# Kernel tuning notes

Measured on AMD Instinct MI355X. Metric: run time of the kernel, lower is better.

Reference implementation:

```python
import jax, jax.numpy as jnp
import numpy as np

EPS_RMS = 1e-8
EPS_LN = 1e-5


def _rms(x):
    return x / jnp.sqrt(jnp.mean(x * x, axis=-1, keepdims=True) + EPS_RMS)


def _ln(x, g, b):
    m = jnp.mean(x, axis=-1, keepdims=True)
    v = jnp.mean((x - m) ** 2, axis=-1, keepdims=True)
    return (x - m) / jnp.sqrt(v + EPS_LN) * g + b


def setup_inputs() -> dict:
    B, S, D, K, V, F = 2, 256, 1024, 8, 32000, 2048
    key = jax.random.key(0)
    ks = jax.random.split(key, 12)
    s = 0.02

    def n(k, shape):
        return jax.random.normal(k, shape, dtype=jnp.float32) * s

    return {
        "x": jax.random.randint(ks[0], (B, S), 0, V),
        "embed_table": n(ks[1], (V, D)),
        "unembed_w": n(ks[2], (V, D)),
        "proj_w": n(ks[3], (K, D, 2 * D)),
        "proj_b": jnp.zeros((K, D), jnp.float32),
        "sa_wv": n(ks[4], (K, D, D)),
        "sa_bv": jnp.zeros((K, D), jnp.float32),
        "sa_wo": n(ks[5], (K, D, D)),
        "sa_bo": jnp.zeros((K, D), jnp.float32),
        "ln1_g": jnp.ones((K, D), jnp.float32),
        "ln1_b": jnp.zeros((K, D), jnp.float32),
        "ca_wv": n(ks[6], (K, D, D)),
        "ca_bv": jnp.zeros((K, D), jnp.float32),
        "ca_wo": n(ks[7], (K, D, D)),
        "ca_bo": jnp.zeros((K, D), jnp.float32),
        "ln2_g": jnp.ones((K, D), jnp.float32),
        "ln2_b": jnp.zeros((K, D), jnp.float32),
        "ff_w1": n(ks[8], (K, F, D)),
        "ff_b1": jnp.zeros((K, F), jnp.float32),
        "ff_w2": n(ks[9], (K, D, F)),
        "ff_b2": jnp.zeros((K, D), jnp.float32),
        "ln3_g": jnp.ones((K, D), jnp.float32),
        "ln3_b": jnp.zeros((K, D), jnp.float32),
    }


def reference(x, embed_table, unembed_w, proj_w, proj_b,
              sa_wv, sa_bv, sa_wo, sa_bo, ln1_g, ln1_b,
              ca_wv, ca_bv, ca_wo, ca_bo, ln2_g, ln2_b,
              ff_w1, ff_b1, ff_w2, ff_b2, ln3_g, ln3_b):
    K = proj_w.shape[0]
    emb = embed_table[x]                      # [B, S, D]
    B, S, D = emb.shape
    I = S - K                                 # number of outer positions (max_i + 1)
    h = emb[:, :I, :]                         # h_prev for all start positions, [B, I, D]
    logits_k = []
    for k in range(K):
        e = emb[:, k + 1:k + 1 + I, :]        # future token embeds for head k
        merged = jnp.concatenate([_rms(h), _rms(e)], axis=-1)   # [B, I, 2D]
        xp = jnp.einsum('bid,ed->bie', merged, proj_w[k]) + proj_b[k]
        # TransformerDecoderLayer on a length-1 sequence: softmax over a single
        # key == 1, so (self-/cross-)attention reduces to out_proj(v_proj(.)).
        sa = (xp @ sa_wv[k].T + sa_bv[k]) @ sa_wo[k].T + sa_bo[k]
        x1 = _ln(xp + sa, ln1_g[k], ln1_b[k])
        ca = (xp @ ca_wv[k].T + ca_bv[k]) @ ca_wo[k].T + ca_bo[k]   # memory = layer input
        x2 = _ln(x1 + ca, ln2_g[k], ln2_b[k])
        ff = jax.nn.relu(x2 @ ff_w1[k].T + ff_b1[k]) @ ff_w2[k].T + ff_b2[k]
        x3 = _ln(x2 + ff, ln3_g[k], ln3_b[k])
        logits_k.append(x3 @ unembed_w.T)     # [B, I, V]
        h = x3
    return jnp.stack(logits_k, axis=2)        # [B, I, K, V]
```

## Files before the change

### kernel.cpp

```cpp
#include <hip/hip_runtime.h>
#include <hip/hip_bf16.h>

#define Dd 1024
#define Ss 256
#define Bz 2
#define Kk 8
#define Vv 32000
#define Ff 2048
#define Ii 248
#define Mm (Bz*Ii)
#define Mp 512
#define Mu (Kk*Mm)
#define Mx 4096

typedef __attribute__((ext_vector_type(8))) short bf16x8_t;
typedef __attribute__((ext_vector_type(4))) float f32x4_t;
typedef __attribute__((ext_vector_type(16))) float f32x16_t;
typedef unsigned long long u64;

__device__ inline ushort f2b(float f) {
    union { float f; unsigned u; } v; v.f = f;
    unsigned u = v.u;
    unsigned r = (u + 0x7fffu + ((u >> 16) & 1u)) >> 16;
    return (ushort)r;
}

__device__ inline void gload16(const void* g, void* l) {
    __builtin_amdgcn_global_load_lds((const __attribute__((address_space(1))) void*)g,
                                     (__attribute__((address_space(3))) void*)l, 16, 0, 0);
}

template<int N> __device__ inline void wait_vmcnt() {
    asm volatile("s_waitcnt vmcnt(%0)" :: "n"(N) : "memory");
}
__device__ inline void bar() {
    asm volatile("" ::: "memory");
    __builtin_amdgcn_s_barrier();
    asm volatile("" ::: "memory");
}

template<int BK>
__device__ inline int swz(int s, int r) {
    if constexpr (BK == 64) return s ^ (r & 7);
    else                    return s ^ ((r >> 1) & 3);
}

__global__ __launch_bounds__(512, 2)
void gemm32(const ushort* __restrict__ A, const ushort* __restrict__ W,
            float* __restrict__ Cf, int Mrows, int KDIM) {
    constexpr int BM = 256, BN = 256, BK = 64, TH = 512, PF = 2;
    constexpr int TILE = (BM + BN) * BK;
    constexpr int ABYTES = BM * BK * 2;
    constexpr int L = (BM + BN) * BK * 2 / (TH * 16);
    __shared__ __align__(16) ushort sm[PF * TILE];

    int bx = blockIdx.x, by = blockIdx.y;
    {
        const int nwg  = gridDim.x * gridDim.y;
        const int orig = by * gridDim.x + bx;
        const int q = nwg >> 3, r = nwg & 7;
        const int xcd = orig & 7, lin = orig >> 3;
        const int wg = (xcd < r ? xcd * (q + 1) : r * (q + 1) + (xcd - r) * q) + lin;
        bx = wg % gridDim.x; by = wg / gridDim.x;
    }
    const int t    = threadIdx.x;
    const int lane = t & 63;
    const int w    = t >> 6;
    const int wr   = (w >> 2) * 128;
    const int wc   = (w & 3) * 64;
    const int tm0  = bx * BM, tn0 = by * BN;

    const ushort* Abase = A + (size_t)tm0 * KDIM;
    const ushort* Wbase = W + (size_t)tn0 * KDIM;

    const ushort* gp[L]; int lo[L];
    #pragma unroll
    for (int j = 0; j < L; ++j) {
        const int i = (t + j * TH) * 16;
        int r, s; const ushort* base;
        if (i < ABYTES) { r = i / (BK * 2); s = (i >> 4) % (BK / 8); base = Abase; }
        else { const int i2 = i - ABYTES; r = i2 / (BK * 2); s = (i2 >> 4) % (BK / 8); base = Wbase; }
        gp[j] = base + (size_t)r * KDIM + (size_t)swz<BK>(s, r) * 8;
        lo[j] = i / 2;
    }
    auto stage = [&](int buf) {
        #pragma unroll
        for (int j = 0; j < L; ++j) gload16(gp[j], &sm[buf * TILE + lo[j]]);
        #pragma unroll
        for (int j = 0; j < L; ++j) gp[j] += BK;
    };

    const int rl = lane & 31, hk = lane >> 5;
    int aoff[4][4], boff[2][4];
    #pragma unroll
    for (int m = 0; m < 4; ++m)
        #pragma unroll
        for (int ks = 0; ks < 4; ++ks) {
            const int r = wr + m * 32 + rl;
            aoff[m][ks] = r * BK + swz<BK>(ks * 2 + hk, r) * 8;
        }
    #pragma unroll
    for (int n = 0; n < 2; ++n)
        #pragma unroll
        for (int ks = 0; ks < 4; ++ks) {
            const int r = wc + n * 32 + rl;
            boff[n][ks] = BM * BK + r * BK + swz<BK>(ks * 2 + hk, r) * 8;
        }

    f32x16_t acc[4][2] = {};
    const int NT = KDIM / BK;

    stage(0); stage(1);
    int buf = 0;
    for (int kt = 0; kt < NT; ++kt) {
        const int remT = NT - 1 - kt;
        if (remT >= 1) wait_vmcnt<L>(); else wait_vmcnt<0>();
        bar();

        const ushort* smb = &sm[buf * TILE];
        #pragma unroll
        for (int ks = 0; ks < 4; ++ks) {
            bf16x8_t af[4], bf[2];
            #pragma unroll
            for (int m = 0; m < 4; ++m) af[m] = *(const bf16x8_t*)&smb[aoff[m][ks]];
            #pragma unroll
            for (int n = 0; n < 2; ++n) bf[n] = *(const bf16x8_t*)&smb[boff[n][ks]];
            #pragma unroll
            for (int m = 0; m < 4; ++m)
                #pragma unroll
                for (int n = 0; n < 2; ++n)
                    acc[m][n] = __builtin_amdgcn_mfma_f32_32x32x16_bf16(af[m], bf[n], acc[m][n], 0, 0, 0);
        }
        bar();
        if (kt + PF < NT) stage(buf);
        buf ^= 1;
    }

    const int cl = lane & 31;
    #pragma unroll
    for (int m = 0; m < 4; ++m)
        #pragma unroll
        for (int n = 0; n < 2; ++n)
            #pragma unroll
            for (int reg = 0; reg < 16; ++reg) {
                const int row = (reg & 3) + 8 * (reg >> 2) + 4 * hk;
                const int r = tm0 + wr + m * 32 + row;
                const int c = tn0 + wc + n * 32 + cl;
                if (r < Mrows) {
                    const int kk  = r / Mm;
                    const int rem = r - kk * Mm;
                    Cf[(size_t)(rem * Kk + kk) * Vv + c] = acc[m][n][reg];
                }
            }
}

template<int BM, int BN, int BK, int TH, int PF, bool RELU, bool UNEMBED>
__global__ __launch_bounds__(TH, 2)
void gemm3(const ushort* __restrict__ A0, const ushort* __restrict__ A1, int lda,
           const ushort* __restrict__ W0, const ushort* __restrict__ W1,
           const float* __restrict__ b0, const float* __restrict__ b1,
           float* __restrict__ Cf0, float* __restrict__ Cf1,
           ushort* __restrict__ Cb0, ushort* __restrict__ Cb1,
           int Mrows, int N, int KDIM) {
    constexpr int NW = TH / 64;
    constexpr int WN = NW / 2;
    constexpr int MR = (BM / 2) / 16;
    constexpr int NR = (BN / WN) / 16;
    constexpr int TILE = (BM + BN) * BK;
    constexpr int ABYTES = BM * BK * 2;
    constexpr int TOT = (BM + BN) * BK * 2;
    constexpr int L = TOT / (TH * 16);
    constexpr int KS = BK / 32;

    __shared__ __align__(16) ushort sm[PF * TILE];

    const ushort* A = A0; const ushort* W = W0; const float* bias = b0;
    float* Cf = Cf0; ushort* Cb = Cb0;
    if (blockIdx.z) { A = A1; W = W1; bias = b1; Cf = Cf1; Cb = Cb1; }

    const int t    = threadIdx.x;
    const int tm0  = blockIdx.x * BM;
    const int tn0  = blockIdx.y * BN;
    const int lane = t & 63;
    const int w    = t >> 6;
    const int wr   = (w / WN) * (BM / 2);
    const int wc   = (w % WN) * (BN / WN);

    const ushort* Abase = A + (size_t)tm0 * lda;
    const ushort* Wbase = W + (size_t)tn0 * KDIM;

    const ushort* gp[L];
    int lo[L];
    #pragma unroll
    for (int j = 0; j < L; ++j) {
        const int i = (t + j * TH) * 16;
        int r, s; const ushort* base; int ld;
        if (i < ABYTES) { r = i / (BK * 2); s = (i >> 4) % (BK / 8); base = Abase; ld = lda; }
        else { const int i2 = i - ABYTES; r = i2 / (BK * 2); s = (i2 >> 4) % (BK / 8); base = Wbase; ld = KDIM; }
        gp[j] = base + (size_t)r * ld + swz<BK>(s, r) * 8;
        lo[j] = i / 2;
    }
    auto stage = [&](int buf) {
        #pragma unroll
        for (int j = 0; j < L; ++j) gload16(gp[j], &sm[buf * TILE + lo[j]]);
        #pragma unroll
        for (int j = 0; j < L; ++j) gp[j] += BK;
    };

    const int h = lane >> 4, rl = lane & 15;
    int aoff[MR][KS], boff[NR][KS];
    #pragma unroll
    for (int m = 0; m < MR; ++m)
        #pragma unroll
        for (int kk = 0; kk < KS; ++kk) {
            const int r = wr + m * 16 + rl;
            aoff[m][kk] = r * BK + swz<BK>(kk * 4 + h, r) * 8;
        }
    #pragma unroll
    for (int n = 0; n < NR; ++n)
        #pragma unroll
        for (int kk = 0; kk < KS; ++kk) {
            const int r = wc + n * 16 + rl;
            boff[n][kk] = BM * BK + r * BK + swz<BK>(kk * 4 + h, r) * 8;
        }

    f32x4_t acc[MR][NR] = {};

    const int NT = KDIM / BK;
    #pragma unroll
    for (int p = 0; p < PF; ++p) stage(p);

    int buf = 0;
    for (int kt = 0; kt < NT; ++kt) {
        const int remT = NT - 1 - kt;
        const int wv = remT < PF - 1 ? remT : PF - 1;
        switch (wv) {
            case 0:  wait_vmcnt<0>();     break;
            case 1:  wait_vmcnt<1 * L>(); break;
            case 2:  wait_vmcnt<2 * L>(); break;
            default: wait_vmcnt<3 * L>(); break;
        }
        bar();

        const ushort* smb = &sm[buf * TILE];
        #pragma unroll
        for (int kk = 0; kk < KS; ++kk) {
            bf16x8_t af[MR], bf[NR];
            #pragma unroll
            for (int m = 0; m < MR; ++m) af[m] = *(const bf16x8_t*)&smb[aoff[m][kk]];
            #pragma unroll
            for (int n = 0; n < NR; ++n) bf[n] = *(const bf16x8_t*)&smb[boff[n][kk]];
            #pragma unroll
            for (int m = 0; m < MR; ++m)
                #pragma unroll
                for (int n = 0; n < NR; ++n)
                    acc[m][n] = __builtin_amdgcn_mfma_f32_16x16x32_bf16(af[m], bf[n], acc[m][n], 0, 0, 0);
        }
        bar();
        if (kt + PF < NT) stage(buf);
        buf = (buf + 1 == PF) ? 0 : buf + 1;
    }

    const int rb = (lane >> 4) * 4;
    const int cl = lane & 15;
    #pragma unroll
    for (int m = 0; m < MR; ++m)
        #pragma unroll
        for (int n = 0; n < NR; ++n)
            #pragma unroll
            for (int i = 0; i < 4; ++i) {
                const int r = tm0 + wr + m * 16 + rb + i;
                const int c = tn0 + wc + n * 16 + cl;
                if (r < Mrows) {
                    float v = acc[m][n][i];
                    if (bias) v += bias[c];
                    if (RELU) v = fmaxf(v, 0.f);
                    if (UNEMBED) {
                        const int kk  = r / Mm;
                        const int rem = r - kk * Mm;
                        Cf[(size_t)(rem * Kk + kk) * Vv + c] = v;
                    } else {
                        if (Cf) Cf[(size_t)r * N + c] = v;
                        if (Cb) Cb[(size_t)r * N + c] = f2b(v);
                    }
                }
            }
}

__global__ __launch_bounds__(256)
void convert_k(const float* __restrict__ src, ushort* __restrict__ dst,
               long n, long perK, long dstPerK, long dstOff) {
    long i = ((long)blockIdx.x * 256 + threadIdx.x) * 4;
    const long stride = (long)gridDim.x * 1024;
    for (; i < n; i += stride) {
        const float4 v = *(const float4*)(src + i);
        const long k = i / perK, rem = i - k * perK;
        ushort4 hh; hh.x = f2b(v.x); hh.y = f2b(v.y); hh.z = f2b(v.z); hh.w = f2b(v.w);
        *(ushort4*)(dst + k * dstPerK + dstOff + rem) = hh;
    }
}

__global__ __launch_bounds__(256)
void copyf_k(const float* __restrict__ src, float* __restrict__ dst,
             long n, long perK, long dstPerK, long dstOff) {
    long i = (long)blockIdx.x * 256 + threadIdx.x;
    const long stride = (long)gridDim.x * 256;
    for (; i < n; i += stride) {
        const long k = i / perK, rem = i - k * perK;
        dst[k * dstPerK + dstOff + rem] = src[i];
    }
}


__global__ __launch_bounds__(256)
void ln12_kernel(const float* __restrict__ sa, const float* __restrict__ xp,
                 const float* __restrict__ ca,
                 const float* __restrict__ g1, const float* __restrict__ b1,
                 const float* __restrict__ g2, const float* __restrict__ b2,
                 float* __restrict__ x2f, ushort* __restrict__ x2b) {
    __shared__ float reds[16];
    const int row = blockIdx.x;
    const int t = threadIdx.x;
    const float4 va = *(const float4*)(sa + (size_t)row * Dd + t * 4);
    const float4 vp = *(const float4*)(xp + (size_t)row * Dd + t * 4);
    float x[4] = { va.x + vp.x, va.y + vp.y, va.z + vp.z, va.w + vp.w };
    float s = x[0] + x[1] + x[2] + x[3];
    float q = x[0]*x[0] + x[1]*x[1] + x[2]*x[2] + x[3]*x[3];
    for (int m = 32; m; m >>= 1) { s += __shfl_xor(s, m); q += __shfl_xor(q, m); }
    if ((t & 63) == 0) { reds[t >> 6] = s; reds[4 + (t >> 6)] = q; }
    __syncthreads();
    s = reds[0] + reds[1] + reds[2] + reds[3];
    q = reds[4] + reds[5] + reds[6] + reds[7];
    float mean = s * (1.f / Dd);
    float rstd = rsqrtf(q * (1.f / Dd) - mean * mean + 1e-5f);
    const float4 vc = *(const float4*)(ca + (size_t)row * Dd + t * 4);
    float y[4];
    #pragma unroll
    for (int j = 0; j < 4; ++j) {
        const int c = t * 4 + j;
        y[j] = (x[j] - mean) * rstd * g1[c] + b1[c] + ((const float*)&vc)[j];
    }
    s = y[0] + y[1] + y[2] + y[3];
    q = y[0]*y[0] + y[1]*y[1] + y[2]*y[2] + y[3]*y[3];
    for (int m = 32; m; m >>= 1) { s += __shfl_xor(s, m); q += __shfl_xor(q, m); }
    if ((t & 63) == 0) { reds[8 + (t >> 6)] = s; reds[12 + (t >> 6)] = q; }
    __syncthreads();
    s = reds[8] + reds[9] + reds[10] + reds[11];
    q = reds[12] + reds[13] + reds[14] + reds[15];
    mean = s * (1.f / Dd);
    rstd = rsqrtf(q * (1.f / Dd) - mean * mean + 1e-5f);
    float z[4]; ushort4 hb;
    #pragma unroll
    for (int j = 0; j < 4; ++j) {
        const int c = t * 4 + j;
        z[j] = (y[j] - mean) * rstd * g2[c] + b2[c];
    }
    hb.x = f2b(z[0]); hb.y = f2b(z[1]); hb.z = f2b(z[2]); hb.w = f2b(z[3]);
    *(float4*)(x2f + (size_t)row * Dd + t * 4) = make_float4(z[0], z[1], z[2], z[3]);
    *(ushort4*)(x2b + (size_t)row * Dd + t * 4) = hb;
}

__global__ __launch_bounds__(256)
void ln3m_kernel(const float* __restrict__ ff, const float* __restrict__ x2,
                 const float* __restrict__ g3, const float* __restrict__ b3,
                 const ushort* __restrict__ remb, ushort* __restrict__ x3k,
                 ushort* __restrict__ merged, int k) {
    __shared__ float reds[12];
    const int r = blockIdx.x;
    const int t = threadIdx.x;
    const int b = r / Ii, i = r - b * Ii;
    const float4 vf = *(const float4*)(ff + (size_t)r * Dd + t * 4);
    const float4 v2 = *(const float4*)(x2 + (size_t)r * Dd + t * 4);
    float x[4] = { vf.x + v2.x, vf.y + v2.y, vf.z + v2.z, vf.w + v2.w };
    float s = x[0] + x[1] + x[2] + x[3];
    float q = x[0]*x[0] + x[1]*x[1] + x[2]*x[2] + x[3]*x[3];
    for (int m = 32; m; m >>= 1) { s += __shfl_xor(s, m); q += __shfl_xor(q, m); }
    if ((t & 63) == 0) { reds[t >> 6] = s; reds[4 + (t >> 6)] = q; }
    __syncthreads();
    s = reds[0] + reds[1] + reds[2] + reds[3];
    q = reds[4] + reds[5] + reds[6] + reds[7];
    const float mean = s * (1.f / Dd);
    const float rstd = rsqrtf(q * (1.f / Dd) - mean * mean + 1e-5f);
    float y[4];
    #pragma unroll
    for (int j = 0; j < 4; ++j) {
        const int c = t * 4 + j;
        y[j] = (x[j] - mean) * rstd * g3[c] + b3[c];
    }
    ushort4 hy; hy.x = f2b(y[0]); hy.y = f2b(y[1]); hy.z = f2b(y[2]); hy.w = f2b(y[3]);
    *(ushort4*)(x3k + (size_t)r * Dd + t * 4) = hy;
    float q2 = y[0]*y[0] + y[1]*y[1] + y[2]*y[2] + y[3]*y[3];
    for (int m = 32; m; m >>= 1) q2 += __shfl_xor(q2, m);
    if ((t & 63) == 0) reds[8 + (t >> 6)] = q2;
    __syncthreads();
    if (k + 1 < Kk) {
        q2 = reds[8] + reds[9] + reds[10] + reds[11];
        const float sc = rsqrtf(q2 * (1.f / Dd) + 1e-8f);
        ushort4 hm; hm.x = f2b(y[0]*sc); hm.y = f2b(y[1]*sc); hm.z = f2b(y[2]*sc); hm.w = f2b(y[3]*sc);
        *(ushort4*)(merged + (size_t)r * (2 * Dd) + t * 4) = hm;
        const ushort4 ev = *(const ushort4*)(remb + (size_t)(b * Ss + k + 2 + i) * Dd + t * 4);
        *(ushort4*)(merged + (size_t)r * (2 * Dd) + Dd + t * 4) = ev;
    }
}

__global__ __launch_bounds__(256)
void gather_rms_merged(const int* __restrict__ xi, const float* __restrict__ table,
                       ushort* __restrict__ remb, ushort* __restrict__ merged) {
    __shared__ float reds[4];
    const int row = blockIdx.x;
    const int t = threadIdx.x;
    const int idx = xi[row];
    const float4 xv = *(const float4*)(table + (size_t)idx * Dd + t * 4);
    float q = xv.x*xv.x + xv.y*xv.y + xv.z*xv.z + xv.w*xv.w;
    for (int m = 32; m; m >>= 1) q += __shfl_xor(q, m);
    if ((t & 63) == 0) reds[t >> 6] = q;
    __syncthreads();
    q = reds[0] + reds[1] + reds[2] + reds[3];
    const float sc = rsqrtf(q * (1.f / Dd) + 1e-8f);
    ushort4 h;
    h.x = f2b(xv.x * sc); h.y = f2b(xv.y * sc); h.z = f2b(xv.z * sc); h.w = f2b(xv.w * sc);
    *(ushort4*)(remb + (size_t)row * Dd + t * 4) = h;
    const int b = row / Ss, s2 = row - b * Ss;
    if (s2 < Ii)
        *(ushort4*)(merged + (size_t)(b * Ii + s2) * (2 * Dd) + t * 4) = h;
    if (s2 >= 1 && s2 <= Ii)
        *(ushort4*)(merged + (size_t)(b * Ii + s2 - 1) * (2 * Dd) + Dd + t * 4) = h;
}


__device__ inline bf16x8_t ld_frag(const ushort* p) {
    union { u64 l[2]; bf16x8_t s; } u;
    u.l[0] = *(const u64*)p;
    u.l[1] = *(const u64*)(p + 4);
    return u.s;
}

#define LDST 40

template<int KDIM, bool RELU, bool UNEMBED>
__global__ __launch_bounds__(256)
void gemm64(const ushort* __restrict__ A, const float* __restrict__ Wt,
            const float* __restrict__ bias, float* __restrict__ Cf,
            ushort* __restrict__ Cb, int Mrows, int N) {
    __shared__ ushort As[64 * LDST];
    __shared__ ushort Ws[64 * LDST];
    const int t    = threadIdx.x;
    const int tm0  = blockIdx.x * 64;
    const int tn0  = blockIdx.y * 64;
    const int lr   = t >> 2;
    const int lc   = (t & 3) * 8;
    const int wid  = t >> 6;
    const int lane = t & 63;
    const int wr   = (wid >> 1) * 32;
    const int wc   = (wid & 1) * 32;
    f32x4_t acc[2][2] = {};
    const bool avalid = (tm0 + lr) < Mrows;
    const ushort* Ap = A  + (size_t)(tm0 + lr) * KDIM + lc;
    const float*  Wp = Wt + (size_t)(tn0 + lr) * KDIM + lc;
    const int aoff = lr * LDST + lc;

    for (int k0 = 0; k0 < KDIM; k0 += 32) {
        union { uint4 qv; u64 l[2]; } av;
        av.qv = make_uint4(0u, 0u, 0u, 0u);
        if (avalid) av.qv = *(const uint4*)(Ap + k0);
        const float4 w0 = *(const float4*)(Wp + k0);
        const float4 w1 = *(const float4*)(Wp + k0 + 4);
        union { ushort us[8]; u64 l[2]; } wb;
        wb.us[0] = f2b(w0.x); wb.us[1] = f2b(w0.y); wb.us[2] = f2b(w0.z); wb.us[3] = f2b(w0.w);
        wb.us[4] = f2b(w1.x); wb.us[5] = f2b(w1.y); wb.us[6] = f2b(w1.z); wb.us[7] = f2b(w1.w);
        __syncthreads();
        *(u64*)&As[aoff]     = av.l[0];
        *(u64*)&As[aoff + 4] = av.l[1];
        *(u64*)&Ws[aoff]     = wb.l[0];
        *(u64*)&Ws[aoff + 4] = wb.l[1];
        __syncthreads();

        const ushort* ab = &As[(wr + (lane & 15)) * LDST + (lane >> 4) * 8];
        const ushort* bb = &Ws[(wc + (lane & 15)) * LDST + (lane >> 4) * 8];
        const bf16x8_t fa0 = ld_frag(ab);
        const bf16x8_t fa1 = ld_frag(ab + 16 * LDST);
        const bf16x8_t fb0 = ld_frag(bb);
        const bf16x8_t fb1 = ld_frag(bb + 16 * LDST);
        acc[0][0] = __builtin_amdgcn_mfma_f32_16x16x32_bf16(fa0, fb0, acc[0][0], 0, 0, 0);
        acc[0][1] = __builtin_amdgcn_mfma_f32_16x16x32_bf16(fa0, fb1, acc[0][1], 0, 0, 0);
        acc[1][0] = __builtin_amdgcn_mfma_f32_16x16x32_bf16(fa1, fb0, acc[1][0], 0, 0, 0);
        acc[1][1] = __builtin_amdgcn_mfma_f32_16x16x32_bf16(fa1, fb1, acc[1][1], 0, 0, 0);
    }

    const int rb = (lane >> 4) * 4;
    const int cl = lane & 15;
    for (int m = 0; m < 2; ++m)
        for (int n = 0; n < 2; ++n)
            for (int i = 0; i < 4; ++i) {
                const int r = tm0 + wr + m * 16 + rb + i;
                const int c = tn0 + wc + n * 16 + cl;
                if (r < Mrows) {
                    float v = acc[m][n][i];
                    if (bias) v += bias[c];
                    if (RELU) v = fmaxf(v, 0.f);
                    if (UNEMBED) {
                        const int kk  = r / Mm;
                        const int rem = r - kk * Mm;
                        Cf[(size_t)(rem * Kk + kk) * Vv + c] = v;
                    } else {
                        if (Cf) Cf[(size_t)r * N + c] = v;
                        if (Cb) Cb[(size_t)r * N + c] = f2b(v);
                    }
                }
            }
}

__global__ __launch_bounds__(256)
void ln_kernel(const float* __restrict__ a, const float* __restrict__ rsd,
               const float* __restrict__ g, const float* __restrict__ bb,
               float* __restrict__ outf, ushort* __restrict__ outb) {
    __shared__ float reds[8];
    const int row = blockIdx.x;
    const int t = threadIdx.x;
    const float4 xa = *(const float4*)(a   + (size_t)row * Dd + t * 4);
    const float4 xr = *(const float4*)(rsd + (size_t)row * Dd + t * 4);
    float x[4] = { xa.x + xr.x, xa.y + xr.y, xa.z + xr.z, xa.w + xr.w };
    float s = x[0] + x[1] + x[2] + x[3];
    float q = x[0]*x[0] + x[1]*x[1] + x[2]*x[2] + x[3]*x[3];
    for (int msk = 32; msk; msk >>= 1) { s += __shfl_xor(s, msk); q += __shfl_xor(q, msk); }
    if ((t & 63) == 0) { reds[t >> 6] = s; reds[4 + (t >> 6)] = q; }
    __syncthreads();
    s = reds[0] + reds[1] + reds[2] + reds[3];
    q = reds[4] + reds[5] + reds[6] + reds[7];
    const float m    = s * (1.f / Dd);
    const float var  = q * (1.f / Dd) - m * m;
    const float rstd = rsqrtf(var + 1e-5f);
    float y[4];
    #pragma unroll
    for (int j = 0; j < 4; ++j) {
        const int c = t * 4 + j;
        y[j] = (x[j] - m) * rstd * g[c] + bb[c];
    }
    if (outf) *(float4*)(outf + (size_t)row * Dd + t * 4) = make_float4(y[0], y[1], y[2], y[3]);
    if (outb) {
        ushort4 h; h.x = f2b(y[0]); h.y = f2b(y[1]); h.z = f2b(y[2]); h.w = f2b(y[3]);
        *(ushort4*)(outb + (size_t)row * Dd + t * 4) = h;
    }
}

__global__ __launch_bounds__(256)
void build_merged(const float* __restrict__ h, const ushort* __restrict__ remb,
                  ushort* __restrict__ merged, int k) {
    __shared__ float reds[4];
    const int r = blockIdx.x;
    const int t = threadIdx.x;
    const int b = r / Ii;
    const int i = r - b * Ii;
    if (k == 0) {
        const ushort4 hv = *(const ushort4*)(remb + (size_t)(b * Ss + i) * Dd + t * 4);
        *(ushort4*)(merged + (size_t)r * (2 * Dd) + t * 4) = hv;
    } else {
        const float4 xv = *(const float4*)(h + (size_t)r * Dd + t * 4);
        float q = xv.x*xv.x + xv.y*xv.y + xv.z*xv.z + xv.w*xv.w;
        for (int msk = 32; msk; msk >>= 1) q += __shfl_xor(q, msk);
        if ((t & 63) == 0) reds[t >> 6] = q;
        __syncthreads();
        q = reds[0] + reds[1] + reds[2] + reds[3];
        const float sc = rsqrtf(q * (1.f / Dd) + 1e-8f);
        ushort4 hv;
        hv.x = f2b(xv.x * sc); hv.y = f2b(xv.y * sc); hv.z = f2b(xv.z * sc); hv.w = f2b(xv.w * sc);
        *(ushort4*)(merged + (size_t)r * (2 * Dd) + t * 4) = hv;
    }
    const ushort4 ev = *(const ushort4*)(remb + (size_t)(b * Ss + k + 1 + i) * Dd + t * 4);
    *(ushort4*)(merged + (size_t)r * (2 * Dd) + Dd + t * 4) = ev;
}

__global__ __launch_bounds__(256)
void gather_rms(const int* __restrict__ xi, const float* __restrict__ table,
                ushort* __restrict__ remb) {
    __shared__ float reds[4];
    const int row = blockIdx.x;
    const int t = threadIdx.x;
    const int idx = xi[row];
    const float4 xv = *(const float4*)(table + (size_t)idx * Dd + t * 4);
    float q = xv.x*xv.x + xv.y*xv.y + xv.z*xv.z + xv.w*xv.w;
    for (int msk = 32; msk; msk >>= 1) q += __shfl_xor(q, msk);
    if ((t & 63) == 0) reds[t >> 6] = q;
    __syncthreads();
    q = reds[0] + reds[1] + reds[2] + reds[3];
    const float sc = rsqrtf(q * (1.f / Dd) + 1e-8f);
    ushort4 h;
    h.x = f2b(xv.x * sc); h.y = f2b(xv.y * sc); h.z = f2b(xv.z * sc); h.w = f2b(xv.w * sc);
    *(ushort4*)(remb + (size_t)row * Dd + t * 4) = h;
}


extern "C" void kernel_launch(void* const* d_in, const int* in_sizes, int n_in,
                              void* d_out, int out_size, void* d_ws, size_t ws_size,
                              hipStream_t stream) {
    const int*   x      = (const int*)  d_in[0];
    const float* table  = (const float*)d_in[1];
    const float* unemb  = (const float*)d_in[2];
    const float* proj_w = (const float*)d_in[3];
    const float* proj_b = (const float*)d_in[4];
    const float* sa_wv  = (const float*)d_in[5];
    const float* sa_bv  = (const float*)d_in[6];
    const float* sa_wo  = (const float*)d_in[7];
    const float* sa_bo  = (const float*)d_in[8];
    const float* ln1_g  = (const float*)d_in[9];
    const float* ln1_b  = (const float*)d_in[10];
    const float* ca_wv  = (const float*)d_in[11];
    const float* ca_bv  = (const float*)d_in[12];
    const float* ca_wo  = (const float*)d_in[13];
    const float* ca_bo  = (const float*)d_in[14];
    const float* ln2_g  = (const float*)d_in[15];
    const float* ln2_b  = (const float*)d_in[16];
    const float* ff_w1  = (const float*)d_in[17];
    const float* ff_b1  = (const float*)d_in[18];
    const float* ff_w2  = (const float*)d_in[19];
    const float* ff_b2  = (const float*)d_in[20];
    const float* ln3_g  = (const float*)d_in[21];
    const float* ln3_b  = (const float*)d_in[22];
    float* out = (float*)d_out;

    char* ws = (char*)d_ws;
    size_t off = 0;
    auto alloc = [&](size_t bytes) -> void* {
        void* p = ws + off;
        off = (off + bytes + 255) & ~(size_t)255;
        return p;
    };

    const size_t NEED = 262100000;

    if (ws_size >= NEED) {
        ushort* wU  = (ushort*)alloc((size_t)Vv * Dd * 2);
        ushort* wP  = (ushort*)alloc((size_t)Kk * Dd * 2 * Dd * 2);
        ushort* wV  = (ushort*)alloc((size_t)Kk * 2 * Dd * Dd * 2);
        ushort* wOs = (ushort*)alloc((size_t)Kk * Dd * Dd * 2);
        ushort* wOc = (ushort*)alloc((size_t)Kk * Dd * Dd * 2);
        ushort* wF1 = (ushort*)alloc((size_t)Kk * Ff * Dd * 2);
        ushort* wF2 = (ushort*)alloc((size_t)Kk * Dd * Ff * 2);
        float*  bV  = (float*) alloc((size_t)Kk * 2 * Dd * 4);
        ushort* remb   = (ushort*)alloc((size_t)Bz * Ss * Dd * 2);
        ushort* merged = (ushort*)alloc((size_t)Mp * 2 * Dd * 2);
        float*  xpf    = (float*) alloc((size_t)Mp * Dd * 4);
        ushort* xpb    = (ushort*)alloc((size_t)Mp * Dd * 2);
        ushort* tb     = (ushort*)alloc((size_t)Mp * 2 * Dd * 2);
        float*  sfa    = (float*) alloc((size_t)Mp * Dd * 4);
        float*  sfc    = (float*) alloc((size_t)Mp * Dd * 4);
        float*  x2f    = (float*) alloc((size_t)Mp * Dd * 4);
        ushort* x2b    = (ushort*)alloc((size_t)Mp * Dd * 2);
        ushort* x3all  = (ushort*)alloc((size_t)Mx * Dd * 2);

        const long nU = (long)Vv * Dd;
        convert_k<<<2048, 256, 0, stream>>>(unemb, wU, nU, nU, nU, 0);
        const long nP = (long)Kk * Dd * 2 * Dd;
        convert_k<<<2048, 256, 0, stream>>>(proj_w, wP, nP, nP, nP, 0);
        const long nDD = (long)Kk * Dd * Dd, pDD = (long)Dd * Dd, pV = 2 * pDD;
        convert_k<<<2048, 256, 0, stream>>>(sa_wv, wV, nDD, pDD, pV, 0);
        convert_k<<<2048, 256, 0, stream>>>(ca_wv, wV, nDD, pDD, pV, pDD);
        convert_k<<<2048, 256, 0, stream>>>(sa_wo, wOs, nDD, nDD, nDD, 0);
        convert_k<<<2048, 256, 0, stream>>>(ca_wo, wOc, nDD, nDD, nDD, 0);
        const long nF = (long)Kk * Ff * Dd;
        convert_k<<<2048, 256, 0, stream>>>(ff_w1, wF1, nF, nF, nF, 0);
        convert_k<<<2048, 256, 0, stream>>>(ff_w2, wF2, nF, nF, nF, 0);
        copyf_k<<<32, 256, 0, stream>>>(sa_bv, bV, (long)Kk * Dd, Dd, 2 * Dd, 0);
        copyf_k<<<32, 256, 0, stream>>>(ca_bv, bV, (long)Kk * Dd, Dd, 2 * Dd, Dd);

        gather_rms_merged<<<Bz * Ss, 256, 0, stream>>>(x, table, remb, merged);

        for (int k = 0; k < Kk; ++k) {
            gemm3<32, 64, 64, 256, 3, false, false><<<dim3(Mp/32, Dd/64, 1), 256, 0, stream>>>(
                merged, merged, 2 * Dd, wP + (size_t)k * Dd * 2 * Dd, wP + (size_t)k * Dd * 2 * Dd,
                proj_b + k * Dd, proj_b + k * Dd, xpf, xpf, xpb, xpb, Mm, Dd, 2 * Dd);
            gemm3<32, 64, 64, 256, 3, false, false><<<dim3(Mp/32, 2*Dd/64, 1), 256, 0, stream>>>(
                xpb, xpb, Dd, wV + (size_t)k * pV, wV + (size_t)k * pV,
                bV + (size_t)k * 2 * Dd, bV + (size_t)k * 2 * Dd,
                nullptr, nullptr, tb, tb, Mm, 2 * Dd, Dd);
            gemm3<32, 64, 64, 256, 3, false, false><<<dim3(Mp/32, Dd/64, 2), 256, 0, stream>>>(
                tb, tb + Dd, 2 * Dd, wOs + (size_t)k * pDD, wOc + (size_t)k * pDD,
                sa_bo + k * Dd, ca_bo + k * Dd, sfa, sfc, nullptr, nullptr, Mm, Dd, Dd);
            ln12_kernel<<<Mm, 256, 0, stream>>>(sfa, xpf, sfc,
                ln1_g + k * Dd, ln1_b + k * Dd, ln2_g + k * Dd, ln2_b + k * Dd, x2f, x2b);
            gemm3<32, 64, 64, 256, 3, true, false><<<dim3(Mp/32, Ff/64, 1), 256, 0, stream>>>(
                x2b, x2b, Dd, wF1 + (size_t)k * Ff * Dd, wF1 + (size_t)k * Ff * Dd,
                ff_b1 + k * Ff, ff_b1 + k * Ff, nullptr, nullptr, tb, tb, Mm, Ff, Dd);
            gemm3<32, 64, 64, 256, 3, false, false><<<dim3(Mp/32, Dd/64, 1), 256, 0, stream>>>(
                tb, tb, Ff, wF2 + (size_t)k * Dd * Ff, wF2 + (size_t)k * Dd * Ff,
                ff_b2 + k * Dd, ff_b2 + k * Dd, sfa, sfa, nullptr, nullptr, Mm, Dd, Ff);
            ln3m_kernel<<<Mm, 256, 0, stream>>>(sfa, x2f, ln3_g + k * Dd, ln3_b + k * Dd,
                remb, x3all + (size_t)k * Mm * Dd, merged, k);
        }

        gemm32<<<dim3(Mx/256, Vv/256, 1), 512, 0, stream>>>(x3all, wU, out, Mu, Dd);
        return;
    }

    ushort* remb   = (ushort*)alloc((size_t)Bz * Ss * Dd * 2);
    ushort* merged = (ushort*)alloc((size_t)Mm * 2 * Dd * 2);
    float*  xpf    = (float*) alloc((size_t)Mm * Dd * 4);
    ushort* xpb    = (ushort*)alloc((size_t)Mm * Dd * 2);
    ushort* tb     = (ushort*)alloc((size_t)Mm * Ff * 2);
    float*  sf     = (float*) alloc((size_t)Mm * Dd * 4);
    float*  x1f    = (float*) alloc((size_t)Mm * Dd * 4);
    float*  x2f    = (float*) alloc((size_t)Mm * Dd * 4);
    ushort* x2b    = (ushort*)alloc((size_t)Mm * Dd * 2);
    float*  hbuf   = (float*) alloc((size_t)Mm * Dd * 4);
    ushort* x3all  = (ushort*)alloc((size_t)Kk * Mm * Dd * 2);

    gather_rms<<<Bz * Ss, 256, 0, stream>>>(x, table, remb);

    const dim3 gD((Mm + 63) / 64, Dd / 64);
    const dim3 gF((Mm + 63) / 64, Ff / 64);
    for (int k = 0; k < Kk; ++k) {
        build_merged<<<Mm, 256, 0, stream>>>(hbuf, remb, merged, k);
        gemm64<2 * Dd, false, false><<<gD, 256, 0, stream>>>(
            merged, proj_w + (size_t)k * Dd * 2 * Dd, proj_b + k * Dd, xpf, xpb, Mm, Dd);
        gemm64<Dd, false, false><<<gD, 256, 0, stream>>>(
            xpb, sa_wv + (size_t)k * Dd * Dd, sa_bv + k * Dd, nullptr, tb, Mm, Dd);
        gemm64<Dd, false, false><<<gD, 256, 0, stream>>>(
            tb, sa_wo + (size_t)k * Dd * Dd, sa_bo + k * Dd, sf, nullptr, Mm, Dd);
        ln_kernel<<<Mm, 256, 0, stream>>>(sf, xpf, ln1_g + k * Dd, ln1_b + k * Dd, x1f, nullptr);
        gemm64<Dd, false, false><<<gD, 256, 0, stream>>>(
            xpb, ca_wv + (size_t)k * Dd * Dd, ca_bv + k * Dd, nullptr, tb, Mm, Dd);
        gemm64<Dd, false, false><<<gD, 256, 0, stream>>>(
            tb, ca_wo + (size_t)k * Dd * Dd, ca_bo + k * Dd, sf, nullptr, Mm, Dd);
        ln_kernel<<<Mm, 256, 0, stream>>>(sf, x1f, ln2_g + k * Dd, ln2_b + k * Dd, x2f, x2b);
        gemm64<Dd, true, false><<<gF, 256, 0, stream>>>(
            x2b, ff_w1 + (size_t)k * Ff * Dd, ff_b1 + k * Ff, nullptr, tb, Mm, Ff);
        gemm64<Ff, false, false><<<gD, 256, 0, stream>>>(
            tb, ff_w2 + (size_t)k * Dd * Ff, ff_b2 + k * Dd, sf, nullptr, Mm, Dd);
        ln_kernel<<<Mm, 256, 0, stream>>>(sf, x2f, ln3_g + k * Dd, ln3_b + k * Dd,
                                          hbuf, x3all + (size_t)k * Mm * Dd);
    }

    const dim3 gU((Kk * Mm) / 64, Vv / 64);
    gemm64<Dd, false, true><<<gU, 256, 0, stream>>>(x3all, unemb, nullptr, out, nullptr, Kk * Mm, Vv);
}
```

Measured before the change: 990.4 us.

## Piggyback weight fp32-to-bf16 conversion as rider blocks on per-layer GEMM launches

```diff
diff --git a/kernel.cpp b/kernel.cpp
--- a/kernel.cpp
+++ b/kernel.cpp
@@ -45,6 +45,163 @@
     else                    return s ^ ((r >> 1) & 3);
 }
 
+#define NTASK 52
+struct CvTab {
+    u64 src[NTASK];
+    u64 dst[NTASK];
+    int start[NTASK + 1];
+    int n;
+};
+
+__device__ inline void run_rider(const CvTab& tab, int g) {
+    int lo = 0;
+    while (lo + 1 < tab.n && tab.start[lo + 1] <= g) ++lo;
+    const float* s = (const float*)tab.src[lo];
+    ushort* d = (ushort*)tab.dst[lo];
+    const long e0 = (long)(g - tab.start[lo]) * 4096 + threadIdx.x * 16;
+    #pragma unroll
+    for (int j = 0; j < 4; ++j) {
+        const float4 v = *(const float4*)(s + e0 + j * 4);
+        ushort4 h; h.x = f2b(v.x); h.y = f2b(v.y); h.z = f2b(v.z); h.w = f2b(v.w);
+        *(ushort4*)(d + e0 + j * 4) = h;
+    }
+}
+
+template<int BM, int BN, int BK, int TH, int PF, int MINW, bool RELU>
+__global__ __launch_bounds__(TH, MINW)
+void gemm3(const ushort* __restrict__ A0, const ushort* __restrict__ A1, int lda,
+           const ushort* __restrict__ W0, const ushort* __restrict__ W1,
+           const float* __restrict__ b0, const float* __restrict__ b1,
+           float* __restrict__ Cf0, float* __restrict__ Cf1,
+           ushort* __restrict__ Cb0, ushort* __restrict__ Cb1,
+           int Mrows, int N, int KDIM,
+           int zChain, CvTab tab, int rBase, int rCnt) {
+    constexpr int NW = TH / 64;
+    constexpr int WN = NW / 2;
+    constexpr int MR = (BM / 2) / 16;
+    constexpr int NR = (BN / WN) / 16;
+    constexpr int TILE = (BM + BN) * BK;
+    constexpr int ABYTES = BM * BK * 2;
+    constexpr int TOT = (BM + BN) * BK * 2;
+    constexpr int L = TOT / (TH * 16);
+    constexpr int KS = BK / 32;
+
+    __shared__ __align__(16) ushort sm[PF * TILE];
+
+    if ((int)blockIdx.z >= zChain) {
+        const int ord = (blockIdx.z - zChain) * (gridDim.x * gridDim.y)
+                      + blockIdx.y * gridDim.x + blockIdx.x;
+        if (ord < rCnt) run_rider(tab, rBase + ord);
+        return;
+    }
+
+    const ushort* A = A0; const ushort* W = W0; const float* bias = b0;
+    float* Cf = Cf0; ushort* Cb = Cb0;
+    if (blockIdx.z) { A = A1; W = W1; bias = b1; Cf = Cf1; Cb = Cb1; }
+
+    const int t    = threadIdx.x;
+    const int tm0  = blockIdx.x * BM;
+    const int tn0  = blockIdx.y * BN;
+    const int lane = t & 63;
+    const int w    = t >> 6;
+    const int wr   = (w / WN) * (BM / 2);
+    const int wc   = (w % WN) * (BN / WN);
+
+    const ushort* Abase = A + (size_t)tm0 * lda;
+    const ushort* Wbase = W + (size_t)tn0 * KDIM;
+
+    const ushort* gp[L];
+    int lo[L];
+    #pragma unroll
+    for (int j = 0; j < L; ++j) {
+        const int i = (t + j * TH) * 16;
+        int r, s; const ushort* base; int ld;
+        if (i < ABYTES) { r = i / (BK * 2); s = (i >> 4) % (BK / 8); base = Abase; ld = lda; }
+        else { const int i2 = i - ABYTES; r = i2 / (BK * 2); s = (i2 >> 4) % (BK / 8); base = Wbase; ld = KDIM; }
+        gp[j] = base + (size_t)r * ld + swz<BK>(s, r) * 8;
+        lo[j] = i / 2;
+    }
+    auto stage = [&](int buf) {
+        #pragma unroll
+        for (int j = 0; j < L; ++j) gload16(gp[j], &sm[buf * TILE + lo[j]]);
+        #pragma unroll
+        for (int j = 0; j < L; ++j) gp[j] += BK;
+    };
+
+    const int h = lane >> 4, rl = lane & 15;
+    int aoff[MR][KS], boff[NR][KS];
+    #pragma unroll
+    for (int m = 0; m < MR; ++m)
+        #pragma unroll
+        for (int kk = 0; kk < KS; ++kk) {
+            const int r = wr + m * 16 + rl;
+            aoff[m][kk] = r * BK + swz<BK>(kk * 4 + h, r) * 8;
+        }
+    #pragma unroll
+    for (int n = 0; n < NR; ++n)
+        #pragma unroll
+        for (int kk = 0; kk < KS; ++kk) {
+            const int r = wc + n * 16 + rl;
+            boff[n][kk] = BM * BK + r * BK + swz<BK>(kk * 4 + h, r) * 8;
+        }
+
+    f32x4_t acc[MR][NR] = {};
+
+    const int NT = KDIM / BK;
+    #pragma unroll
+    for (int p = 0; p < PF; ++p) stage(p);
+
+    int buf = 0;
+    for (int kt = 0; kt < NT; ++kt) {
+        const int remT = NT - 1 - kt;
+        const int wv = remT < PF - 1 ? remT : PF - 1;
+        switch (wv) {
+            case 0:  wait_vmcnt<0>();     break;
+            case 1:  wait_vmcnt<1 * L>(); break;
+            case 2:  wait_vmcnt<2 * L>(); break;
+            default: wait_vmcnt<3 * L>(); break;
+        }
+        bar();
+
+        const ushort* smb = &sm[buf * TILE];
+        #pragma unroll
+        for (int kk = 0; kk < KS; ++kk) {
+            bf16x8_t af[MR], bf[NR];
+            #pragma unroll
+            for (int m = 0; m < MR; ++m) af[m] = *(const bf16x8_t*)&smb[aoff[m][kk]];
+            #pragma unroll
+            for (int n = 0; n < NR; ++n) bf[n] = *(const bf16x8_t*)&smb[boff[n][kk]];
+            #pragma unroll
+            for (int m = 0; m < MR; ++m)
+                #pragma unroll
+                for (int n = 0; n < NR; ++n)
+                    acc[m][n] = __builtin_amdgcn_mfma_f32_16x16x32_bf16(af[m], bf[n], acc[m][n], 0, 0, 0);
+        }
+        bar();
+        if (kt + PF < NT) stage(buf);
+        buf = (buf + 1 == PF) ? 0 : buf + 1;
+    }
+
+    const int rb = (lane >> 4) * 4;
+    const int cl = lane & 15;
+    #pragma unroll
+    for (int m = 0; m < MR; ++m)
+        #pragma unroll
+        for (int n = 0; n < NR; ++n)
+            #pragma unroll
+            for (int i = 0; i < 4; ++i) {
+                const int r = tm0 + wr + m * 16 + rb + i;
+                const int c = tn0 + wc + n * 16 + cl;
+                if (r < Mrows) {
+                    float v = acc[m][n][i];
+                    if (bias) v += bias[c];
+                    if (RELU) v = fmaxf(v, 0.f);
+                    if (Cf) Cf[(size_t)r * N + c] = v;
+                    if (Cb) Cb[(size_t)r * N + c] = f2b(v);
+                }
+            }
+}
+
 __global__ __launch_bounds__(512, 2)
 void gemm32(const ushort* __restrict__ A, const ushort* __restrict__ W,
             float* __restrict__ Cf, int Mrows, int KDIM) {
@@ -150,139 +307,6 @@
                     const int kk  = r / Mm;
                     const int rem = r - kk * Mm;
                     Cf[(size_t)(rem * Kk + kk) * Vv + c] = acc[m][n][reg];
-                }
-            }
-}
-
-template<int BM, int BN, int BK, int TH, int PF, bool RELU, bool UNEMBED>
-__global__ __launch_bounds__(TH, 2)
-void gemm3(const ushort* __restrict__ A0, const ushort* __restrict__ A1, int lda,
-           const ushort* __restrict__ W0, const ushort* __restrict__ W1,
-           const float* __restrict__ b0, const float* __restrict__ b1,
-           float* __restrict__ Cf0, float* __restrict__ Cf1,
-           ushort* __restrict__ Cb0, ushort* __restrict__ Cb1,
-           int Mrows, int N, int KDIM) {
-    constexpr int NW = TH / 64;
-    constexpr int WN = NW / 2;
-    constexpr int MR = (BM / 2) / 16;
-    constexpr int NR = (BN / WN) / 16;
-    constexpr int TILE = (BM + BN) * BK;
-    constexpr int ABYTES = BM * BK * 2;
-    constexpr int TOT = (BM + BN) * BK * 2;
-    constexpr int L = TOT / (TH * 16);
-    constexpr int KS = BK / 32;
-
-    __shared__ __align__(16) ushort sm[PF * TILE];
-
-    const ushort* A = A0; const ushort* W = W0; const float* bias = b0;
-    float* Cf = Cf0; ushort* Cb = Cb0;
-    if (blockIdx.z) { A = A1; W = W1; bias = b1; Cf = Cf1; Cb = Cb1; }
-
-    const int t    = threadIdx.x;
-    const int tm0  = blockIdx.x * BM;
-    const int tn0  = blockIdx.y * BN;
-    const int lane = t & 63;
-    const int w    = t >> 6;
-    const int wr   = (w / WN) * (BM / 2);
-    const int wc   = (w % WN) * (BN / WN);
-
-    const ushort* Abase = A + (size_t)tm0 * lda;
-    const ushort* Wbase = W + (size_t)tn0 * KDIM;
-
-    const ushort* gp[L];
-    int lo[L];
-    #pragma unroll
-    for (int j = 0; j < L; ++j) {
-        const int i = (t + j * TH) * 16;
-        int r, s; const ushort* base; int ld;
-        if (i < ABYTES) { r = i / (BK * 2); s = (i >> 4) % (BK / 8); base = Abase; ld = lda; }
-        else { const int i2 = i - ABYTES; r = i2 / (BK * 2); s = (i2 >> 4) % (BK / 8); base = Wbase; ld = KDIM; }
-        gp[j] = base + (size_t)r * ld + swz<BK>(s, r) * 8;
-        lo[j] = i / 2;
-    }
-    auto stage = [&](int buf) {
-        #pragma unroll
-        for (int j = 0; j < L; ++j) gload16(gp[j], &sm[buf * TILE + lo[j]]);
-        #pragma unroll
-        for (int j = 0; j < L; ++j) gp[j] += BK;
-    };
-
-    const int h = lane >> 4, rl = lane & 15;
-    int aoff[MR][KS], boff[NR][KS];
-    #pragma unroll
-    for (int m = 0; m < MR; ++m)
-        #pragma unroll
-        for (int kk = 0; kk < KS; ++kk) {
-            const int r = wr + m * 16 + rl;
-            aoff[m][kk] = r * BK + swz<BK>(kk * 4 + h, r) * 8;
-        }
-    #pragma unroll
-    for (int n = 0; n < NR; ++n)
-        #pragma unroll
-        for (int kk = 0; kk < KS; ++kk) {
-            const int r = wc + n * 16 + rl;
-            boff[n][kk] = BM * BK + r * BK + swz<BK>(kk * 4 + h, r) * 8;
-        }
-
-    f32x4_t acc[MR][NR] = {};
-
-    const int NT = KDIM / BK;
-    #pragma unroll
-    for (int p = 0; p < PF; ++p) stage(p);
-
-    int buf = 0;
-    for (int kt = 0; kt < NT; ++kt) {
-        const int remT = NT - 1 - kt;
-        const int wv = remT < PF - 1 ? remT : PF - 1;
-        switch (wv) {
-            case 0:  wait_vmcnt<0>();     break;
-            case 1:  wait_vmcnt<1 * L>(); break;
-            case 2:  wait_vmcnt<2 * L>(); break;
-            default: wait_vmcnt<3 * L>(); break;
-        }
-        bar();
-
-        const ushort* smb = &sm[buf * TILE];
-        #pragma unroll
-        for (int kk = 0; kk < KS; ++kk) {
-            bf16x8_t af[MR], bf[NR];
-            #pragma unroll
-            for (int m = 0; m < MR; ++m) af[m] = *(const bf16x8_t*)&smb[aoff[m][kk]];
-            #pragma unroll
-            for (int n = 0; n < NR; ++n) bf[n] = *(const bf16x8_t*)&smb[boff[n][kk]];
-            #pragma unroll
-            for (int m = 0; m < MR; ++m)
-                #pragma unroll
-                for (int n = 0; n < NR; ++n)
-                    acc[m][n] = __builtin_amdgcn_mfma_f32_16x16x32_bf16(af[m], bf[n], acc[m][n], 0, 0, 0);
-        }
-        bar();
-        if (kt + PF < NT) stage(buf);
-        buf = (buf + 1 == PF) ? 0 : buf + 1;
-    }
-
-    const int rb = (lane >> 4) * 4;
-    const int cl = lane & 15;
-    #pragma unroll
-    for (int m = 0; m < MR; ++m)
-        #pragma unroll
-        for (int n = 0; n < NR; ++n)
-            #pragma unroll
-            for (int i = 0; i < 4; ++i) {
-                const int r = tm0 + wr + m * 16 + rb + i;
-                const int c = tn0 + wc + n * 16 + cl;
-                if (r < Mrows) {
-                    float v = acc[m][n][i];
-                    if (bias) v += bias[c];
-                    if (RELU) v = fmaxf(v, 0.f);
-                    if (UNEMBED) {
-                        const int kk  = r / Mm;
-                        const int rem = r - kk * Mm;
-                        Cf[(size_t)(rem * Kk + kk) * Vv + c] = v;
-                    } else {
-                        if (Cf) Cf[(size_t)r * N + c] = v;
-                        if (Cb) Cb[(size_t)r * N + c] = f2b(v);
-                    }
                 }
             }
 }
@@ -629,14 +653,15 @@
     const size_t NEED = 262100000;
 
     if (ws_size >= NEED) {
-        ushort* wU  = (ushort*)alloc((size_t)Vv * Dd * 2);
-        ushort* wP  = (ushort*)alloc((size_t)Kk * Dd * 2 * Dd * 2);
-        ushort* wV  = (ushort*)alloc((size_t)Kk * 2 * Dd * Dd * 2);
-        ushort* wOs = (ushort*)alloc((size_t)Kk * Dd * Dd * 2);
-        ushort* wOc = (ushort*)alloc((size_t)Kk * Dd * Dd * 2);
-        ushort* wF1 = (ushort*)alloc((size_t)Kk * Ff * Dd * 2);
-        ushort* wF2 = (ushort*)alloc((size_t)Kk * Dd * Ff * 2);
-        float*  bV  = (float*) alloc((size_t)Kk * 2 * Dd * 4);
+        ushort* wU   = (ushort*)alloc((size_t)Vv * Dd * 2);
+        ushort* wP   = (ushort*)alloc((size_t)Kk * Dd * 2 * Dd * 2);
+        ushort* wVsa = (ushort*)alloc((size_t)Kk * Dd * Dd * 2);
+        ushort* wVca = (ushort*)alloc((size_t)Kk * Dd * Dd * 2);
+        ushort* wOs  = (ushort*)alloc((size_t)Kk * Dd * Dd * 2);
+        ushort* wOc  = (ushort*)alloc((size_t)Kk * Dd * Dd * 2);
+        ushort* wF1  = (ushort*)alloc((size_t)Kk * Ff * Dd * 2);
+        ushort* wF2  = (ushort*)alloc((size_t)Kk * Dd * Ff * 2);
+        float*  bV   = (float*) alloc((size_t)Kk * 2 * Dd * 4);
         ushort* remb   = (ushort*)alloc((size_t)Bz * Ss * Dd * 2);
         ushort* merged = (ushort*)alloc((size_t)Mp * 2 * Dd * 2);
         float*  xpf    = (float*) alloc((size_t)Mp * Dd * 4);
@@ -648,42 +673,77 @@
         ushort* x2b    = (ushort*)alloc((size_t)Mp * Dd * 2);
         ushort* x3all  = (ushort*)alloc((size_t)Mx * Dd * 2);
 
-        const long nU = (long)Vv * Dd;
-        convert_k<<<2048, 256, 0, stream>>>(unemb, wU, nU, nU, nU, 0);
-        const long nP = (long)Kk * Dd * 2 * Dd;
-        convert_k<<<2048, 256, 0, stream>>>(proj_w, wP, nP, nP, nP, 0);
-        const long nDD = (long)Kk * Dd * Dd, pDD = (long)Dd * Dd, pV = 2 * pDD;
-        convert_k<<<2048, 256, 0, stream>>>(sa_wv, wV, nDD, pDD, pV, 0);
-        convert_k<<<2048, 256, 0, stream>>>(ca_wv, wV, nDD, pDD, pV, pDD);
-        convert_k<<<2048, 256, 0, stream>>>(sa_wo, wOs, nDD, nDD, nDD, 0);
-        convert_k<<<2048, 256, 0, stream>>>(ca_wo, wOc, nDD, nDD, nDD, 0);
-        const long nF = (long)Kk * Ff * Dd;
-        convert_k<<<2048, 256, 0, stream>>>(ff_w1, wF1, nF, nF, nF, 0);
-        convert_k<<<2048, 256, 0, stream>>>(ff_w2, wF2, nF, nF, nF, 0);
+        const long pP  = (long)Dd * 2 * Dd;
+        const long pDD = (long)Dd * Dd;
+        const long pF  = (long)Ff * Dd;
+
+        CvTab tab; int cum = 0; tab.n = 0;
+        auto addTask = [&](const float* s, ushort* d, long elems) {
+            tab.src[tab.n] = (u64)s; tab.dst[tab.n] = (u64)d;
+            tab.start[tab.n] = cum; cum += (int)(elems / 4096); tab.n++;
+        };
+        for (int k = 1; k < Kk; ++k) {
+            addTask(proj_w + (size_t)k * pP, wP  + (size_t)k * pP, pP);
+            addTask(sa_wv + (size_t)k * pDD, wVsa + (size_t)k * pDD, pDD);
+            addTask(ca_wv + (size_t)k * pDD, wVca + (size_t)k * pDD, pDD);
+            addTask(sa_wo + (size_t)k * pDD, wOs + (size_t)k * pDD, pDD);
+            addTask(ca_wo + (size_t)k * pDD, wOc + (size_t)k * pDD, pDD);
+            addTask(ff_w1 + (size_t)k * pF, wF1 + (size_t)k * pF, pF);
+            addTask(ff_w2 + (size_t)k * pF, wF2 + (size_t)k * pF, pF);
+        }
+        addTask(unemb, wU, (long)Vv * Dd);
+        tab.start[tab.n] = cum;
+        const int totC = cum;
+        int rPos = 0;
+        auto riders = [&](int plane, int zChain, int& base, int& cnt) -> int {
+            base = rPos;
+            int want = totC - rPos; if (want > 768) want = 768;
+            cnt = want; rPos += want;
+            const int planes = (want + plane - 1) / plane;
+            return zChain + planes;
+        };
+
+        convert_k<<<512, 256, 0, stream>>>(proj_w, wP, pP, pP, pP, 0);
+        convert_k<<<512, 256, 0, stream>>>(sa_wv, wVsa, pDD, pDD, pDD, 0);
+        convert_k<<<512, 256, 0, stream>>>(ca_wv, wVca, pDD, pDD, pDD, 0);
+        convert_k<<<512, 256, 0, stream>>>(sa_wo, wOs, pDD, pDD, pDD, 0);
+        convert_k<<<512, 256, 0, stream>>>(ca_wo, wOc, pDD, pDD, pDD, 0);
+        convert_k<<<512, 256, 0, stream>>>(ff_w1, wF1, pF, pF, pF, 0);
+        convert_k<<<512, 256, 0, stream>>>(ff_w2, wF2, pF, pF, pF, 0);
         copyf_k<<<32, 256, 0, stream>>>(sa_bv, bV, (long)Kk * Dd, Dd, 2 * Dd, 0);
         copyf_k<<<32, 256, 0, stream>>>(ca_bv, bV, (long)Kk * Dd, Dd, 2 * Dd, Dd);
-
         gather_rms_merged<<<Bz * Ss, 256, 0, stream>>>(x, table, remb, merged);
 
+        int rb_, rc_, zg;
         for (int k = 0; k < Kk; ++k) {
-            gemm3<32, 64, 64, 256, 3, false, false><<<dim3(Mp/32, Dd/64, 1), 256, 0, stream>>>(
-                merged, merged, 2 * Dd, wP + (size_t)k * Dd * 2 * Dd, wP + (size_t)k * Dd * 2 * Dd,
-                proj_b + k * Dd, proj_b + k * Dd, xpf, xpf, xpb, xpb, Mm, Dd, 2 * Dd);
-            gemm3<32, 64, 64, 256, 3, false, false><<<dim3(Mp/32, 2*Dd/64, 1), 256, 0, stream>>>(
-                xpb, xpb, Dd, wV + (size_t)k * pV, wV + (size_t)k * pV,
-                bV + (size_t)k * 2 * Dd, bV + (size_t)k * 2 * Dd,
-                nullptr, nullptr, tb, tb, Mm, 2 * Dd, Dd);
-            gemm3<32, 64, 64, 256, 3, false, false><<<dim3(Mp/32, Dd/64, 2), 256, 0, stream>>>(
+            zg = riders(16 * 16, 1, rb_, rc_);
+            gemm3<32, 64, 64, 256, 3, 2, false><<<dim3(Mp/32, Dd/64, zg), 256, 0, stream>>>(
+                merged, merged, 2 * Dd, wP + (size_t)k * pP, wP + (size_t)k * pP,
+                proj_b + k * Dd, proj_b + k * Dd, xpf, xpf, xpb, xpb, Mm, Dd, 2 * Dd,
+                1, tab, rb_, rc_);
+            zg = riders(16 * 16, 2, rb_, rc_);
+            gemm3<32, 64, 64, 256, 3, 2, false><<<dim3(Mp/32, Dd/64, zg), 256, 0, stream>>>(
+                xpb, xpb, Dd, wVsa + (size_t)k * pDD, wVca + (size_t)k * pDD,
+                bV + (size_t)k * 2 * Dd, bV + (size_t)k * 2 * Dd + Dd,
+                nullptr, nullptr, tb, tb + Dd, Mm, 2 * Dd, Dd,
+                2, tab, rb_, rc_);
+            zg = riders(16 * 16, 2, rb_, rc_);
+            gemm3<32, 64, 64, 256, 3, 2, false><<<dim3(Mp/32, Dd/64, zg), 256, 0, stream>>>(
                 tb, tb + Dd, 2 * Dd, wOs + (size_t)k * pDD, wOc + (size_t)k * pDD,
-                sa_bo + k * Dd, ca_bo + k * Dd, sfa, sfc, nullptr, nullptr, Mm, Dd, Dd);
+                sa_bo + k * Dd, ca_bo + k * Dd, sfa, sfc, nullptr, nullptr, Mm, Dd, Dd,
+                2, tab, rb_, rc_);
             ln12_kernel<<<Mm, 256, 0, stream>>>(sfa, xpf, sfc,
                 ln1_g + k * Dd, ln1_b + k * Dd, ln2_g + k * Dd, ln2_b + k * Dd, x2f, x2b);
-            gemm3<32, 64, 64, 256, 3, true, false><<<dim3(Mp/32, Ff/64, 1), 256, 0, stream>>>(
-                x2b, x2b, Dd, wF1 + (size_t)k * Ff * Dd, wF1 + (size_t)k * Ff * Dd,
-                ff_b1 + k * Ff, ff_b1 + k * Ff, nullptr, nullptr, tb, tb, Mm, Ff, Dd);
-            gemm3<32, 64, 64, 256, 3, false, false><<<dim3(Mp/32, Dd/64, 1), 256, 0, stream>>>(
-                tb, tb, Ff, wF2 + (size_t)k * Dd * Ff, wF2 + (size_t)k * Dd * Ff,
-                ff_b2 + k * Dd, ff_b2 + k * Dd, sfa, sfa, nullptr, nullptr, Mm, Dd, Ff);
+            zg = riders(16 * 32, 1, rb_, rc_);
+            gemm3<32, 64, 64, 256, 3, 2, true><<<dim3(Mp/32, Ff/64, zg), 256, 0, stream>>>(
+                x2b, x2b, Dd, wF1 + (size_t)k * pF, wF1 + (size_t)k * pF,
+                ff_b1 + k * Ff, ff_b1 + k * Ff, nullptr, nullptr, tb, tb, Mm, Ff, Dd,
+                1, tab, rb_, rc_);
+            zg = riders(16 * 16, 1, rb_, rc_);
+            gemm3<32, 64, 64, 256, 3, 2, false><<<dim3(Mp/32, Dd/64, zg), 256, 0, stream>>>(
+                tb, tb, Ff, wF2 + (size_t)k * pF, wF2 + (size_t)k * pF,
+                ff_b2 + k * Dd, ff_b2 + k * Dd, sfa, sfa, nullptr, nullptr, Mm, Dd, Ff,
+                1, tab, rb_, rc_);
             ln3m_kernel<<<Mm, 256, 0, stream>>>(sfa, x2f, ln3_g + k * Dd, ln3_b + k * Dd,
                 remb, x3all + (size_t)k * Mm * Dd, merged, k);
         }
```

After: 1.038 ms. 4.8% more time.
